# Performance work log

Measured on AMD Instinct MI355X. Metric: run time of the kernel, lower is better.

The kernel has to match this reference:

```python
import jax, jax.numpy as jnp
import numpy as np

B, H, C, LB, PW = 8192, 128, 1, 64, 32
WL = LB + PW


def setup_inputs() -> dict:
    key = jax.random.key(0)
    ks = jax.random.split(key, 9)
    inv_sqrt_h = 1.0 / np.sqrt(H)
    return {
        "x": jax.random.normal(ks[0], (B, LB, 1), jnp.float32),
        # per-step Linear weights for F (hidden->hidden) and H (hidden->target)
        "F_w": jax.random.normal(ks[1], (WL, H, H), jnp.float32) * inv_sqrt_h,
        "F_b": jax.random.normal(ks[2], (WL, H), jnp.float32) * 0.05,
        "H_w": jax.random.normal(ks[3], (WL, C, H), jnp.float32) * inv_sqrt_h,
        "H_b": jax.random.normal(ks[4], (WL, C), jnp.float32) * 0.05,
        "init_state": jax.random.normal(ks[5], (H,), jnp.float32),
        # well-conditioned covariance / noise params so inv(S) is stable
        "init_cov": jnp.eye(H, dtype=jnp.float32) + 0.02 * jax.random.normal(ks[6], (H, H), jnp.float32),
        "Q": 0.1 * jnp.eye(H, dtype=jnp.float32) + 0.01 * jax.random.normal(ks[7], (H, H), jnp.float32),
        "R": 0.1 * jnp.eye(C, dtype=jnp.float32) + 0.01 * jax.random.normal(ks[8], (C, C), jnp.float32),
    }


def _kalman_forward(x, F_w, F_b, H_w, H_b, init_state, init_cov, Q, R):
    b = x.shape[0]
    h = init_state.shape[0]
    I = jnp.eye(h, dtype=x.dtype)
    hs0 = jnp.broadcast_to(init_state, (b, h))
    P0 = jnp.broadcast_to(init_cov, (b, h, h))
    obs = jnp.moveaxis(x[:, :LB, :C], 0, 1)  # (LB, B, C)

    def filt_step(carry, inp):
        hs, P = carry
        Fw, Fb, Hw, Hb, y = inp
        hs_pred = hs @ Fw.T + Fb                                   # (B, h)
        P_pred = jnp.einsum('ij,bjk,lk->bil', Fw, P, Fw) + Q       # (B, h, h)
        y_pred = hs_pred @ Hw.T + Hb                               # (B, c)
        resid = y - y_pred
        S = jnp.einsum('ij,bjk,lk->bil', Hw, P_pred, Hw) + R       # (B, c, c)
        PHt = jnp.einsum('bij,kj->bik', P_pred, Hw)                # (B, h, c)
        K = PHt @ jnp.linalg.inv(S)                                # (B, h, c)
        hs_new = hs_pred + jnp.einsum('bhc,bc->bh', K, resid)
        P_new = (I - jnp.einsum('bhc,ck->bhk', K, Hw)) @ P_pred
        return (hs_new, P_new), None

    (hs, _), _ = jax.lax.scan(
        filt_step, (hs0, P0), (F_w[:LB], F_b[:LB], H_w[:LB], H_b[:LB], obs))

    def pred_step(hs, inp):
        Fw, Fb, Hw, Hb = inp
        hs = hs @ Fw.T + Fb
        em = hs @ Hw.T + Hb                                        # (B, c)
        return hs, em

    _, ems = jax.lax.scan(pred_step, hs, (F_w[LB:], F_b[LB:], H_w[LB:], H_b[LB:]))
    # ems: (PW, B, C) -> torch.cat(dim=1) order -> (B, PW*C) -> unsqueeze(-1)
    out = jnp.moveaxis(ems, 0, 1).reshape(b, PW * C)
    return out[..., None]


def reference(x, F_w, F_b, H_w, H_b, init_state, init_cov, Q, R):
    return _kalman_forward(x, F_w, F_b, H_w, H_b, init_state, init_cov, Q, R)
```

## Files before the change

kernel.cpp:

```cpp
#include <hip/hip_runtime.h>

#define NB 8192
#define NH 128
#define NLB 64
#define NPW 32
#define MAGIC 1234567
#define SP 136

typedef __attribute__((ext_vector_type(8))) __bf16 bf16x8;
typedef __attribute__((ext_vector_type(4))) __bf16 bf16x4;
typedef __attribute__((ext_vector_type(4))) float f32x4;

__device__ __forceinline__ f32x4 mfma3(bf16x8 ah, bf16x8 al, bf16x8 bh, bf16x8 bl, f32x4 c) {
    c = __builtin_amdgcn_mfma_f32_16x16x32_bf16(ah, bh, c, 0, 0, 0);
    c = __builtin_amdgcn_mfma_f32_16x16x32_bf16(ah, bl, c, 0, 0, 0);
    c = __builtin_amdgcn_mfma_f32_16x16x32_bf16(al, bh, c, 0, 0, 0);
    return c;
}

__device__ __forceinline__ void ld_split8(const float* p, bf16x8& h, bf16x8& l) {
    float vv[8];
    *(float4*)vv       = *(const float4*)p;
    *(float4*)(vv + 4) = *(const float4*)(p + 4);
#pragma unroll
    for (int j = 0; j < 8; ++j) {
        __bf16 t = (__bf16)vv[j];
        h[j] = t;
        l[j] = (__bf16)(vv[j] - (float)t);
    }
}

#define KT_OFF   560
#define g63_OFF  (KT_OFF + 8192)
#define MR_OFF   (g63_OFF + 128)
#define DV_OFF   (MR_OFF + 2048)
#define DP_OFF   (DV_OFF + 32)
#define UV_OFF   (DP_OFF + 32)
#define SINK_OFF 32000
#define FLAG_I   34000
#define FHI_OFF  40960
#define FLO_OFF  (FHI_OFF + 524288)
#define WS_SPLIT_BYTES  ((size_t)(FLO_OFF + 524288) * 4)

#define DYN_LDS  ((144 + 144 + 128 + 128) * SP * 2)

__global__ __launch_bounds__(256)
void k0_split(const float* __restrict__ F, float* __restrict__ ws)
{
    size_t e = ((size_t)blockIdx.x * 256 + threadIdx.x) * 8;
    __bf16* fh = (__bf16*)(ws + FHI_OFF);
    __bf16* fl = (__bf16*)(ws + FLO_OFF);
    float v[8];
    *(float4*)v       = *(const float4*)(F + e);
    *(float4*)(v + 4) = *(const float4*)(F + e + 4);
    bf16x8 h, l;
#pragma unroll
    for (int j = 0; j < 8; ++j) {
        __bf16 t = (__bf16)v[j];
        h[j] = t;
        l[j] = (__bf16)(v[j] - (float)t);
    }
    *(bf16x8*)&fh[e] = h;
    *(bf16x8*)&fl[e] = l;
}

__global__ __launch_bounds__(1024, 4)
void k1_recur(const float* __restrict__ Fw,
              const float* __restrict__ Fb,
              const float* __restrict__ Hw,
              const float* __restrict__ Hb,
              const float* __restrict__ init_state,
              const float* __restrict__ init_cov,
              const float* __restrict__ Qm,
              const float* __restrict__ Rm,
              float* __restrict__ ws,
              int use_split)
{
    const int tid = threadIdx.x;
    const int wg  = blockIdx.x;
    int* wsl = (int*)ws;

    extern __shared__ __align__(16) char dsm[];
    __bf16* PhiS = (__bf16*)dsm;
    __bf16* PloS = PhiS + 144 * SP;
    __bf16* UhiS = PloS + 144 * SP;
    __bf16* UloS = UhiS + 128 * SP;

    __shared__ float smisc[1280];
    __shared__ float shH[NH], shK[NH], shW[NH], shV[NH], shFV[NH], shFW[NH], shG[NH], shGn[NH];
    __shared__ float scal[16];

    float* pV = smisc;
    float* pW = smisc + 640;

    if (wg == 0) {
        const float Rv = Rm[0];
        const int lane = tid & 63, w = tid >> 6;
        const int lm = lane & 15, kg = lane >> 4;
        const int a = w >> 2, b = w & 3;
        const int arow = a * 32, bcol = b * 32;

#pragma unroll
        for (int ii = 0; ii < 16; ++ii) {
            int e = tid + ii * 1024;
            int r = e >> 7, c = e & 127;
            float v = init_cov[e];
            __bf16 h = (__bf16)v;
            PhiS[r * SP + c] = h;
            PloS[r * SP + c] = (__bf16)(v - (float)h);
        }
#pragma unroll
        for (int ii = 0; ii < 2; ++ii) {
            int e = tid + ii * 1024;
            int r = 128 + (e >> 7), c = e & 127;
            float v = (r == 130) ? init_state[c] : 0.f;
            __bf16 h = (__bf16)v;
            PhiS[r * SP + c] = h;
            PloS[r * SP + c] = (__bf16)(v - (float)h);
        }
        if (tid < NH) shG[tid] = init_state[tid];
        if (tid == 0) scal[1] = 0.f;
        __syncthreads();

        for (int t = 0; t < NLB; ++t) {
            if (tid < NH) shH[tid] = Hw[t * NH + tid];
            bf16x8 fbH[2][4], fbL[2][4];
            if (use_split) {
                const __bf16* fh = (const __bf16*)(ws + FHI_OFF) + (size_t)t * 16384;
                const __bf16* fl = (const __bf16*)(ws + FLO_OFF) + (size_t)t * 16384;
#pragma unroll
                for (int rs = 0; rs < 2; ++rs)
#pragma unroll
                    for (int kc = 0; kc < 4; ++kc) {
                        int ro = (bcol + rs * 16 + lm) * 128 + kc * 32 + kg * 8;
                        fbH[rs][kc] = *(const bf16x8*)&fh[ro];
                        fbL[rs][kc] = *(const bf16x8*)&fl[ro];
                    }
            } else {
                const float* Ft = Fw + (size_t)t * 16384;
#pragma unroll
                for (int rs = 0; rs < 2; ++rs)
#pragma unroll
                    for (int kc = 0; kc < 4; ++kc)
                        ld_split8(Ft + (bcol + rs * 16 + lm) * 128 + kc * 32 + kg * 8,
                                  fbH[rs][kc], fbL[rs][kc]);
            }

            const f32x4 zero4 = {0.f, 0.f, 0.f, 0.f};
            f32x4 accU[2][2];
#pragma unroll
            for (int rt = 0; rt < 2; ++rt)
#pragma unroll
                for (int ct = 0; ct < 2; ++ct) accU[rt][ct] = zero4;
#pragma unroll
            for (int kc = 0; kc < 4; ++kc) {
#pragma unroll
                for (int rt = 0; rt < 2; ++rt) {
                    bf16x8 ph = *(bf16x8*)&PhiS[(arow + rt * 16 + lm) * SP + kc * 32 + kg * 8];
                    bf16x8 pl = *(bf16x8*)&PloS[(arow + rt * 16 + lm) * SP + kc * 32 + kg * 8];
#pragma unroll
                    for (int ct = 0; ct < 2; ++ct)
                        accU[rt][ct] = mfma3(ph, pl, fbH[ct][kc], fbL[ct][kc], accU[rt][ct]);
                }
            }
            if (a == 0) {
                f32x4 accV[2];
                accV[0] = zero4; accV[1] = zero4;
#pragma unroll
                for (int kc = 0; kc < 4; ++kc) {
                    bf16x8 vh = *(bf16x8*)&PhiS[(128 + lm) * SP + kc * 32 + kg * 8];
                    bf16x8 vl = *(bf16x8*)&PloS[(128 + lm) * SP + kc * 32 + kg * 8];
#pragma unroll
                    for (int ct = 0; ct < 2; ++ct)
                        accV[ct] = mfma3(vh, vl, fbH[ct][kc], fbL[ct][kc], accV[ct]);
                }
                if (kg == 0) {
#pragma unroll
                    for (int ct = 0; ct < 2; ++ct) {
                        int c = bcol + ct * 16 + lm;
                        shFW[c] = accV[ct][0];
                        shFV[c] = accV[ct][1];
                        shGn[c] = accV[ct][2];
                    }
                }
            }
#pragma unroll
            for (int rt = 0; rt < 2; ++rt)
#pragma unroll
                for (int ct = 0; ct < 2; ++ct) {
                    int Urow = arow + rt * 16 + kg * 4;
                    int Ucol = bcol + ct * 16 + lm;
                    bf16x4 uh, ul;
#pragma unroll
                    for (int reg = 0; reg < 4; ++reg) {
                        float v = accU[rt][ct][reg];
                        __bf16 h = (__bf16)v;
                        uh[reg] = h;
                        ul[reg] = (__bf16)(v - (float)h);
                    }
                    *(bf16x4*)&UhiS[Ucol * SP + Urow] = uh;
                    *(bf16x4*)&UloS[Ucol * SP + Urow] = ul;
                }
            __syncthreads();

            if (tid < NH) shG[tid] = shGn[tid] + shFV[tid] * scal[1] + Fb[t * NH + tid];
            f32x4 accP[2][2];
#pragma unroll
            for (int rt2 = 0; rt2 < 2; ++rt2)
#pragma unroll
                for (int ct2 = 0; ct2 < 2; ++ct2)
#pragma unroll
                    for (int reg = 0; reg < 4; ++reg)
                        accP[rt2][ct2][reg] =
                            Qm[(bcol + rt2 * 16 + kg * 4 + reg) * 128 + arow + ct2 * 16 + lm];
#pragma unroll
            for (int kc = 0; kc < 4; ++kc) {
#pragma unroll
                for (int ct2 = 0; ct2 < 2; ++ct2) {
                    bf16x8 uh = *(bf16x8*)&UhiS[(arow + ct2 * 16 + lm) * SP + kc * 32 + kg * 8];
                    bf16x8 ul = *(bf16x8*)&UloS[(arow + ct2 * 16 + lm) * SP + kc * 32 + kg * 8];
#pragma unroll
                    for (int rt2 = 0; rt2 < 2; ++rt2)
                        accP[rt2][ct2] = mfma3(fbH[rt2][kc], fbL[rt2][kc], uh, ul, accP[rt2][ct2]);
                }
            }
            {
                float vacc[2][4];
#pragma unroll
                for (int i = 0; i < 2; ++i)
#pragma unroll
                    for (int j = 0; j < 4; ++j) vacc[i][j] = 0.f;
                float wp[2] = {0.f, 0.f};
#pragma unroll
                for (int rt2 = 0; rt2 < 2; ++rt2)
#pragma unroll
                    for (int ct2 = 0; ct2 < 2; ++ct2) {
                        int c = arow + ct2 * 16 + lm;
                        float hc = shH[c], fwc = shFW[c];
#pragma unroll
                        for (int reg = 0; reg < 4; ++reg) {
                            int r = bcol + rt2 * 16 + kg * 4 + reg;
                            float val = accP[rt2][ct2][reg] - shFV[r] * fwc;
                            __bf16 vh = (__bf16)val;
                            PhiS[r * SP + c] = vh;
                            PloS[r * SP + c] = (__bf16)(val - (float)vh);
                            vacc[rt2][reg] += val * hc;
                            wp[ct2] += val * shH[r];
                        }
                    }
#pragma unroll
                for (int off = 1; off < 16; off <<= 1)
#pragma unroll
                    for (int rt2 = 0; rt2 < 2; ++rt2)
#pragma unroll
                        for (int reg = 0; reg < 4; ++reg)
                            vacc[rt2][reg] += __shfl_xor(vacc[rt2][reg], off);
                if (lm == 0)
#pragma unroll
                    for (int rt2 = 0; rt2 < 2; ++rt2)
#pragma unroll
                        for (int reg = 0; reg < 4; ++reg)
                            pV[(bcol + rt2 * 16 + kg * 4 + reg) * 5 + a] = vacc[rt2][reg];
#pragma unroll
                for (int ct2 = 0; ct2 < 2; ++ct2) {
                    wp[ct2] += __shfl_xor(wp[ct2], 16);
                    wp[ct2] += __shfl_xor(wp[ct2], 32);
                }
                if (kg == 0)
#pragma unroll
                    for (int ct2 = 0; ct2 < 2; ++ct2)
                        pW[(arow + ct2 * 16 + lm) * 5 + b] = wp[ct2];
            }
            __syncthreads();

            if (tid < 128) {
                shV[tid] = pV[tid * 5] + pV[tid * 5 + 1] + pV[tid * 5 + 2] + pV[tid * 5 + 3];
            } else if (tid < 256) {
                int c = tid - 128;
                shW[c] = pW[c * 5] + pW[c * 5 + 1] + pW[c * 5 + 2] + pW[c * 5 + 3];
            } else if (tid < 320) {
                int l = tid - 256;
                float A0 = pV[10 * l]     + pV[10 * l + 1] + pV[10 * l + 2] + pV[10 * l + 3];
                float A1 = pV[10 * l + 5] + pV[10 * l + 6] + pV[10 * l + 7] + pV[10 * l + 8];
                float a_ = shH[2 * l] * A0 + shH[2 * l + 1] * A1;
#pragma unroll
                for (int off = 32; off; off >>= 1) a_ += __shfl_down(a_, off);
                if (l == 0) scal[0] = 1.f / (Rv + a_);
            } else if (tid < 384) {
                int l = tid - 320;
                float a_ = shH[l] * shG[l] + shH[l + 64] * shG[l + 64];
#pragma unroll
                for (int off = 32; off; off >>= 1) a_ += __shfl_down(a_, off);
                if (l == 0) scal[1] = -(a_ + Hb[t]);
            }
            __syncthreads();

            if (tid < 128) {
                float k = shV[tid] * scal[0];
                shK[tid] = k;
                ws[KT_OFF + t * 128 + tid] = k;
                float w3[3] = { shW[tid], k, shG[tid] };
#pragma unroll
                for (int rr = 0; rr < 3; ++rr) {
                    __bf16 h = (__bf16)w3[rr];
                    PhiS[(128 + rr) * SP + tid] = h;
                    PloS[(128 + rr) * SP + tid] = (__bf16)(w3[rr] - (float)h);
                }
            }
            __syncthreads();
        }

        if (tid < 128) ws[g63_OFF + tid] = shG[tid] + shK[tid] * scal[1];
        __syncthreads();
        if (tid == 0) {
            __threadfence();
            __atomic_store_n(&wsl[FLAG_I + 0], MAGIC, __ATOMIC_RELEASE);
        }
        return;
    }

    if (wg <= 32) {
        const int pt = 63 + wg;
        float* part = smisc;
        float* shU  = shV;
        if (tid < NH) shU[tid] = Hw[pt * NH + tid];
        if (tid == 0) scal[2] = Hb[pt];
        __syncthreads();

        for (int j = pt; j >= NLB; --j) {
            const float* Fj  = Fw + (size_t)j * 16384;
            const float* fbj = Fb + j * NH;
            if (tid < 64) {
                float a = shU[tid] * fbj[tid] + shU[tid + 64] * fbj[tid + 64];
#pragma unroll
                for (int off = 32; off; off >>= 1) a += __shfl_down(a, off);
                if (tid == 0) scal[2] += a;
            }
            {
                const int c = tid & 127, sgc = tid >> 7;
                float a = 0.f;
                const float* base = Fj + (size_t)(sgc * 16) * 128 + c;
#pragma unroll 4
                for (int i = 0; i < 16; ++i) a += shU[sgc * 16 + i] * base[(size_t)i * 128];
                part[c * 9 + sgc] = a;
            }
            __syncthreads();
            if (tid < 128) {
                float a = 0.f;
#pragma unroll
                for (int s = 0; s < 8; ++s) a += part[tid * 9 + s];
                shU[tid] = a;
            }
            __syncthreads();
        }

        if (tid < NH) ws[UV_OFF + (wg - 1) * NH + tid] = shU[tid];
        if (tid == 0) ws[DP_OFF + (wg - 1)] = scal[2];
        __syncthreads();
        if (tid == 0) {
            __threadfence();
            __atomic_store_n(&wsl[FLAG_I + wg * 16], MAGIC, __ATOMIC_RELEASE);
        }
        return;
    }

    {
        if (tid >= 256) return;
        const int lane = tid & 63;
        float r0 = 1.f + (float)tid * 1e-6f + (float)wg * 1e-5f;
        while (true) {
#pragma unroll 8
            for (int i = 0; i < 4096; ++i) r0 = __builtin_fmaf(r0, 0.99999988f, 1.0e-7f);
            int done = 0;
            if (lane == 0) {
                int cnt = 0;
                for (int w2 = 0; w2 <= 32; ++w2)
                    cnt += (__atomic_load_n(&wsl[FLAG_I + w2 * 16], __ATOMIC_RELAXED) == MAGIC);
                done = (cnt == 33) ? 1 : 0;
            }
            done = __shfl(done, 0);
            if (done) break;
        }
        if (r0 == 123.4567f) ws[SINK_OFF + wg] = r0;
    }
}

__global__ __launch_bounds__(256)
void k2_cols(const float* __restrict__ Fw,
             const float* __restrict__ Hw,
             float* __restrict__ ws)
{
    const int tid = threadIdx.x;
    const int c   = blockIdx.x;
    __shared__ float shX[128], shY[128], p2[256], pu[32 * 9];
    __shared__ float sc[1];

    if (c == 64) {
        int p = tid >> 3, sg = tid & 7;
        float a = 0.f;
#pragma unroll
        for (int i = 0; i < 16; ++i)
            a += ws[UV_OFF + p * 128 + sg * 16 + i] * ws[g63_OFF + sg * 16 + i];
        pu[p * 9 + sg] = a;
        __syncthreads();
        if (tid < 32) {
            float d = ws[DP_OFF + tid];
#pragma unroll
            for (int s = 0; s < 8; ++s) d += pu[tid * 9 + s];
            ws[DV_OFF + tid] = d;
        }
        return;
    }

    if (tid < 128) shX[tid] = ws[KT_OFF + c * 128 + tid];
    __syncthreads();

    for (int j = c + 1; j < NLB; ++j) {
        const float* Fj = Fw + (size_t)j * 16384;
        {
            int r = tid & 127, sg = tid >> 7;
            float a = 0.f;
            const float4* fr = (const float4*)(Fj + r * 128 + sg * 64);
#pragma unroll
            for (int q = 0; q < 16; ++q) {
                float4 f = fr[q];
                int m = sg * 64 + q * 4;
                a += f.x * shX[m] + f.y * shX[m+1] + f.z * shX[m+2] + f.w * shX[m+3];
            }
            p2[sg * 128 + r] = a;
        }
        __syncthreads();
        if (tid < 128) shY[tid] = p2[tid] + p2[128 + tid];
        __syncthreads();
        if (tid < 64) {
            float a = Hw[j * 128 + 2*tid] * shY[2*tid] + Hw[j * 128 + 2*tid + 1] * shY[2*tid + 1];
#pragma unroll
            for (int off = 32; off; off >>= 1) a += __shfl_down(a, off);
            if (tid == 0) sc[0] = a;
        }
        __syncthreads();
        if (tid < 128) shX[tid] = shY[tid] - ws[KT_OFF + j * 128 + tid] * sc[0];
        __syncthreads();
    }

    {
        int p = tid >> 3, sg = tid & 7;
        float a = 0.f;
#pragma unroll
        for (int i = 0; i < 16; ++i)
            a += ws[UV_OFF + p * 128 + sg * 16 + i] * shX[sg * 16 + i];
        pu[p * 9 + sg] = a;
        __syncthreads();
        if (tid < 32) {
            float a = 0.f;
#pragma unroll
            for (int s = 0; s < 8; ++s) a += pu[tid * 9 + s];
            ws[MR_OFF + tid * 64 + c] = a;
        }
    }
}

__global__ __launch_bounds__(1024)
void k3_batch(const float* __restrict__ x,
              const float* __restrict__ ws,
              float* __restrict__ out)
{
    const int tid = threadIdx.x;
    const int wgb = blockIdx.x;
    __shared__ float Ml[NPW * 65];
    __shared__ float dl[NPW];

#pragma unroll
    for (int ii = 0; ii < 2; ++ii) {
        int idx = tid + ii * 1024;
        int p = idx >> 6, n = idx & 63;
        Ml[p * 65 + n] = ws[MR_OFF + p * 64 + n];
    }
    if (tid < NPW) dl[tid] = ws[DV_OFF + tid];
    __syncthreads();

    const int r  = wgb * 256 + (tid >> 2);
    const int pg = tid & 3;
    float acc[8];
#pragma unroll
    for (int pi = 0; pi < 8; ++pi) acc[pi] = dl[pg * 8 + pi];
    const float4* xr = (const float4*)(x + (size_t)r * 64);
#pragma unroll
    for (int c4 = 0; c4 < 16; ++c4) {
        float4 xv = xr[c4];
#pragma unroll
        for (int pi = 0; pi < 8; ++pi) {
            const float* mrow = &Ml[(pg * 8 + pi) * 65 + c4 * 4];
            acc[pi] += xv.x * mrow[0] + xv.y * mrow[1] + xv.z * mrow[2] + xv.w * mrow[3];
        }
    }
    float* op = out + (size_t)r * 32 + pg * 8;
    *(float4*)op       = make_float4(acc[0], acc[1], acc[2], acc[3]);
    *(float4*)(op + 4) = make_float4(acc[4], acc[5], acc[6], acc[7]);
}

extern "C" void kernel_launch(void* const* d_in, const int* in_sizes, int n_in,
                              void* d_out, int out_size, void* d_ws, size_t ws_size,
                              hipStream_t stream) {
    const float* x          = (const float*)d_in[0];
    const float* F_w        = (const float*)d_in[1];
    const float* F_b        = (const float*)d_in[2];
    const float* H_w        = (const float*)d_in[3];
    const float* H_b        = (const float*)d_in[4];
    const float* init_state = (const float*)d_in[5];
    const float* init_cov   = (const float*)d_in[6];
    const float* Qm         = (const float*)d_in[7];
    const float* Rm         = (const float*)d_in[8];
    float* ws   = (float*)d_ws;
    float* outp = (float*)d_out;

    int use_split = (ws_size >= WS_SPLIT_BYTES + 65536) ? 1 : 0;

    (void)hipFuncSetAttribute((const void*)k1_recur,
                              hipFuncAttributeMaxDynamicSharedMemorySize, DYN_LDS);

    if (use_split)
        k0_split<<<dim3(512), dim3(256), 0, stream>>>(F_w, ws);
    k1_recur<<<dim3(256), dim3(1024), DYN_LDS, stream>>>(
        F_w, F_b, H_w, H_b, init_state, init_cov, Qm, Rm, ws, use_split);
    k2_cols<<<dim3(65), dim3(256), 0, stream>>>(F_w, H_w, ws);
    k3_batch<<<dim3(32), dim3(1024), 0, stream>>>(x, ws, outp);
}
```

Before: 1.304 ms.

## Restructure Kalman recurrence step to cut barriers and vectorize covariance stores

In the serial filter workgroup, Q is now loaded into registers once before the time loop instead of being reloaded every step. The MFMA operand order is swapped so each lane holds a row-contiguous fragment, which lets covariance stores and FW/H reads use 4-wide LDS accesses. The gain and scalar reductions are merged into one phase, removing a __syncthreads per step on the latency-bound 64-step chain. The spinning helper workgroups now poll more often and stop after a bounded number of rounds. The main risk is changed reduction order and LDS bank patterns in the transposed layout.

```diff
diff --git a/kernel.cpp b/kernel.cpp
--- a/kernel.cpp
+++ b/kernel.cpp
@@ -64,7 +64,7 @@
     *(bf16x8*)&fl[e] = l;
 }
 
-__global__ __launch_bounds__(1024, 4)
+__global__ __launch_bounds__(1024) __attribute__((amdgpu_waves_per_eu(4, 4)))
 void k1_recur(const float* __restrict__ Fw,
               const float* __restrict__ Fb,
               const float* __restrict__ Hw,
@@ -87,7 +87,9 @@
     __bf16* UloS = UhiS + 128 * SP;
 
     __shared__ float smisc[1280];
-    __shared__ float shH[NH], shK[NH], shW[NH], shV[NH], shFV[NH], shFW[NH], shG[NH], shGn[NH];
+    __shared__ __align__(16) float shH[NH];
+    __shared__ __align__(16) float shFW[NH];
+    __shared__ float shK[NH], shV[NH], shFV[NH], shG[NH], shGn[NH];
     __shared__ float scal[16];
 
     float* pV = smisc;
@@ -120,6 +122,14 @@
         }
         if (tid < NH) shG[tid] = init_state[tid];
         if (tid == 0) scal[1] = 0.f;
+
+        f32x4 qreg[2][2];
+#pragma unroll
+        for (int rt2 = 0; rt2 < 2; ++rt2)
+#pragma unroll
+            for (int ct2 = 0; ct2 < 2; ++ct2)
+                qreg[rt2][ct2] =
+                    *(const f32x4*)&Qm[(bcol + rt2 * 16 + lm) * 128 + arow + ct2 * 16 + kg * 4];
         __syncthreads();
 
         for (int t = 0; t < NLB; ++t) {
@@ -203,16 +213,11 @@
                 }
             __syncthreads();
 
-            if (tid < NH) shG[tid] = shGn[tid] + shFV[tid] * scal[1] + Fb[t * NH + tid];
             f32x4 accP[2][2];
 #pragma unroll
             for (int rt2 = 0; rt2 < 2; ++rt2)
 #pragma unroll
-                for (int ct2 = 0; ct2 < 2; ++ct2)
-#pragma unroll
-                    for (int reg = 0; reg < 4; ++reg)
-                        accP[rt2][ct2][reg] =
-                            Qm[(bcol + rt2 * 16 + kg * 4 + reg) * 128 + arow + ct2 * 16 + lm];
+                for (int ct2 = 0; ct2 < 2; ++ct2) accP[rt2][ct2] = qreg[rt2][ct2];
 #pragma unroll
             for (int kc = 0; kc < 4; ++kc) {
 #pragma unroll
@@ -221,91 +226,107 @@
                     bf16x8 ul = *(bf16x8*)&UloS[(arow + ct2 * 16 + lm) * SP + kc * 32 + kg * 8];
 #pragma unroll
                     for (int rt2 = 0; rt2 < 2; ++rt2)
-                        accP[rt2][ct2] = mfma3(fbH[rt2][kc], fbL[rt2][kc], uh, ul, accP[rt2][ct2]);
+                        accP[rt2][ct2] = mfma3(uh, ul, fbH[rt2][kc], fbL[rt2][kc], accP[rt2][ct2]);
                 }
             }
             {
-                float vacc[2][4];
+                float vr[2] = {0.f, 0.f};
+                float wc[2][4];
 #pragma unroll
                 for (int i = 0; i < 2; ++i)
 #pragma unroll
-                    for (int j = 0; j < 4; ++j) vacc[i][j] = 0.f;
-                float wp[2] = {0.f, 0.f};
-#pragma unroll
-                for (int rt2 = 0; rt2 < 2; ++rt2)
+                    for (int j = 0; j < 4; ++j) wc[i][j] = 0.f;
+#pragma unroll
+                for (int rt2 = 0; rt2 < 2; ++rt2) {
+                    int R = bcol + rt2 * 16 + lm;
+                    float fvr = shFV[R];
+                    float hr  = shH[R];
 #pragma unroll
                     for (int ct2 = 0; ct2 < 2; ++ct2) {
-                        int c = arow + ct2 * 16 + lm;
-                        float hc = shH[c], fwc = shFW[c];
+                        int cb = arow + ct2 * 16 + kg * 4;
+                        f32x4 fw4 = *(const f32x4*)&shFW[cb];
+                        f32x4 h4  = *(const f32x4*)&shH[cb];
+                        bf16x4 ph4, pl4;
 #pragma unroll
                         for (int reg = 0; reg < 4; ++reg) {
-                            int r = bcol + rt2 * 16 + kg * 4 + reg;
-                            float val = accP[rt2][ct2][reg] - shFV[r] * fwc;
+                            float val = accP[rt2][ct2][reg] - fvr * fw4[reg];
                             __bf16 vh = (__bf16)val;
-                            PhiS[r * SP + c] = vh;
-                            PloS[r * SP + c] = (__bf16)(val - (float)vh);
-                            vacc[rt2][reg] += val * hc;
-                            wp[ct2] += val * shH[r];
+                            ph4[reg] = vh;
+                            pl4[reg] = (__bf16)(val - (float)vh);
+                            vr[rt2]      += val * h4[reg];
+                            wc[ct2][reg] += val * hr;
                         }
+                        *(bf16x4*)&PhiS[R * SP + cb] = ph4;
+                        *(bf16x4*)&PloS[R * SP + cb] = pl4;
                     }
-#pragma unroll
-                for (int off = 1; off < 16; off <<= 1)
+                }
+#pragma unroll
+                for (int rt2 = 0; rt2 < 2; ++rt2) {
+                    vr[rt2] += __shfl_xor(vr[rt2], 16);
+                    vr[rt2] += __shfl_xor(vr[rt2], 32);
+                }
+                if (kg == 0)
 #pragma unroll
                     for (int rt2 = 0; rt2 < 2; ++rt2)
+                        pV[(bcol + rt2 * 16 + lm) * 5 + a] = vr[rt2];
+#pragma unroll
+                for (int ct2 = 0; ct2 < 2; ++ct2)
+#pragma unroll
+                    for (int reg = 0; reg < 4; ++reg) {
+#pragma unroll
+                        for (int off = 1; off < 16; off <<= 1)
+                            wc[ct2][reg] += __shfl_xor(wc[ct2][reg], off);
+                    }
+                if (lm == 0)
+#pragma unroll
+                    for (int ct2 = 0; ct2 < 2; ++ct2)
 #pragma unroll
                         for (int reg = 0; reg < 4; ++reg)
-                            vacc[rt2][reg] += __shfl_xor(vacc[rt2][reg], off);
-                if (lm == 0)
-#pragma unroll
-                    for (int rt2 = 0; rt2 < 2; ++rt2)
-#pragma unroll
-                        for (int reg = 0; reg < 4; ++reg)
-                            pV[(bcol + rt2 * 16 + kg * 4 + reg) * 5 + a] = vacc[rt2][reg];
-#pragma unroll
-                for (int ct2 = 0; ct2 < 2; ++ct2) {
-                    wp[ct2] += __shfl_xor(wp[ct2], 16);
-                    wp[ct2] += __shfl_xor(wp[ct2], 32);
-                }
-                if (kg == 0)
-#pragma unroll
-                    for (int ct2 = 0; ct2 < 2; ++ct2)
-                        pW[(arow + ct2 * 16 + lm) * 5 + b] = wp[ct2];
+                            pW[(arow + ct2 * 16 + kg * 4 + reg) * 5 + b] = wc[ct2][reg];
+            }
+            if (tid < NH) {
+                float g = shGn[tid] + shFV[tid] * scal[1] + Fb[t * NH + tid];
+                shG[tid] = g;
+                __bf16 h = (__bf16)g;
+                PhiS[130 * SP + tid] = h;
+                PloS[130 * SP + tid] = (__bf16)(g - (float)h);
             }
             __syncthreads();
 
-            if (tid < 128) {
-                shV[tid] = pV[tid * 5] + pV[tid * 5 + 1] + pV[tid * 5 + 2] + pV[tid * 5 + 3];
-            } else if (tid < 256) {
-                int c = tid - 128;
-                shW[c] = pW[c * 5] + pW[c * 5 + 1] + pW[c * 5 + 2] + pW[c * 5 + 3];
-            } else if (tid < 320) {
-                int l = tid - 256;
-                float A0 = pV[10 * l]     + pV[10 * l + 1] + pV[10 * l + 2] + pV[10 * l + 3];
-                float A1 = pV[10 * l + 5] + pV[10 * l + 6] + pV[10 * l + 7] + pV[10 * l + 8];
-                float a_ = shH[2 * l] * A0 + shH[2 * l + 1] * A1;
-#pragma unroll
-                for (int off = 32; off; off >>= 1) a_ += __shfl_down(a_, off);
-                if (l == 0) scal[0] = 1.f / (Rv + a_);
-            } else if (tid < 384) {
-                int l = tid - 320;
-                float a_ = shH[l] * shG[l] + shH[l + 64] * shG[l + 64];
-#pragma unroll
-                for (int off = 32; off; off >>= 1) a_ += __shfl_down(a_, off);
-                if (l == 0) scal[1] = -(a_ + Hb[t]);
-            }
-            __syncthreads();
-
-            if (tid < 128) {
-                float k = shV[tid] * scal[0];
-                shK[tid] = k;
-                ws[KT_OFF + t * 128 + tid] = k;
-                float w3[3] = { shW[tid], k, shG[tid] };
-#pragma unroll
-                for (int rr = 0; rr < 3; ++rr) {
-                    __bf16 h = (__bf16)w3[rr];
-                    PhiS[(128 + rr) * SP + tid] = h;
-                    PloS[(128 + rr) * SP + tid] = (__bf16)(w3[rr] - (float)h);
-                }
+            if (tid < 64) {
+                int j0 = tid, j1 = tid + 64;
+                float v0 = pV[j0 * 5] + pV[j0 * 5 + 1] + pV[j0 * 5 + 2] + pV[j0 * 5 + 3];
+                float v1 = pV[j1 * 5] + pV[j1 * 5 + 1] + pV[j1 * 5 + 2] + pV[j1 * 5 + 3];
+                float p = shH[j0] * v0 + shH[j1] * v1;
+#pragma unroll
+                for (int off = 1; off < 64; off <<= 1) p += __shfl_xor(p, off);
+                float s = 1.f / (Rv + p);
+                float k0 = v0 * s, k1v = v1 * s;
+                shK[j0] = k0; shK[j1] = k1v;
+                ws[KT_OFF + t * 128 + j0] = k0;
+                ws[KT_OFF + t * 128 + j1] = k1v;
+                __bf16 h0 = (__bf16)k0;
+                PhiS[129 * SP + j0] = h0;
+                PloS[129 * SP + j0] = (__bf16)(k0 - (float)h0);
+                __bf16 h1 = (__bf16)k1v;
+                PhiS[129 * SP + j1] = h1;
+                PloS[129 * SP + j1] = (__bf16)(k1v - (float)h1);
+            } else if (tid < 128) {
+                int c0 = tid - 64, c1 = tid;
+                float w0 = pW[c0 * 5] + pW[c0 * 5 + 1] + pW[c0 * 5 + 2] + pW[c0 * 5 + 3];
+                float w1 = pW[c1 * 5] + pW[c1 * 5 + 1] + pW[c1 * 5 + 2] + pW[c1 * 5 + 3];
+                __bf16 h0 = (__bf16)w0;
+                PhiS[128 * SP + c0] = h0;
+                PloS[128 * SP + c0] = (__bf16)(w0 - (float)h0);
+                __bf16 h1 = (__bf16)w1;
+                PhiS[128 * SP + c1] = h1;
+                PloS[128 * SP + c1] = (__bf16)(w1 - (float)h1);
+            } else if (tid < 192) {
+                int l = tid - 128;
+                float p = shH[l] * shG[l] + shH[l + 64] * shG[l + 64];
+#pragma unroll
+                for (int off = 1; off < 64; off <<= 1) p += __shfl_xor(p, off);
+                if (l == 0) scal[1] = -(p + Hb[t]);
             }
             __syncthreads();
         }
@@ -368,9 +389,10 @@
         if (tid >= 256) return;
         const int lane = tid & 63;
         float r0 = 1.f + (float)tid * 1e-6f + (float)wg * 1e-5f;
+        int rounds = 0;
         while (true) {
 #pragma unroll 8
-            for (int i = 0; i < 4096; ++i) r0 = __builtin_fmaf(r0, 0.99999988f, 1.0e-7f);
+            for (int i = 0; i < 1024; ++i) r0 = __builtin_fmaf(r0, 0.99999988f, 1.0e-7f);
             int done = 0;
             if (lane == 0) {
                 int cnt = 0;
@@ -379,7 +401,7 @@
                 done = (cnt == 33) ? 1 : 0;
             }
             done = __shfl(done, 0);
-            if (done) break;
+            if (done || ++rounds > 4096) break;
         }
         if (r0 == 123.4567f) ws[SINK_OFF + wg] = r0;
     }
```

New measurement: 1.167 ms. 10.5% less time.
